# Kernel tuning notes

Measured on AMD Instinct MI355X. Metric: run time of the kernel, lower is better.

The kernel has to match this reference:

```python
import jax, jax.numpy as jnp
import numpy as np

B, S, D = 8, 1024, 768
H = 12
HD = D // H
DROPOUT_P = 0.5


def setup_inputs() -> dict:
    key = jax.random.key(0)
    ks = jax.random.split(key, 9)
    scale = 1.0 / np.sqrt(D)
    return {
        "x": jax.random.normal(ks[0], (B, S, D), dtype=jnp.float32),
        "wq": jax.random.normal(ks[1], (D, D), dtype=jnp.float32) * scale,
        "bq": jax.random.normal(ks[2], (D,), dtype=jnp.float32) * 0.01,
        "wk": jax.random.normal(ks[3], (D, D), dtype=jnp.float32) * scale,
        "bk": jax.random.normal(ks[4], (D,), dtype=jnp.float32) * 0.01,
        "wv": jax.random.normal(ks[5], (D, D), dtype=jnp.float32) * scale,
        "bv": jax.random.normal(ks[6], (D,), dtype=jnp.float32) * 0.01,
        "wo": jax.random.normal(ks[7], (D, D), dtype=jnp.float32) * scale,
        "bo": jax.random.normal(ks[8], (D,), dtype=jnp.float32) * 0.01,
    }


def reference(x, wq, bq, wk, bk, wv, bv, wo, bo):
    # QKV projections (torch Linear: y = x @ W.T + b)
    def proj(w, b):
        y = jnp.einsum("bsd,ed->bse", x, w) + b
        # [B,S,D] -> [B,H,S,HD]
        return y.reshape(B, S, H, HD).transpose(0, 2, 1, 3)

    q = proj(wq, bq)
    k = proj(wk, bk)
    v = proj(wv, bv)

    scores = jnp.einsum("bhqd,bhkd->bhqk", q, k) / jnp.sqrt(
        jnp.asarray(HD, dtype=x.dtype)
    )
    # dropout BEFORE softmax (non-standard, faithful to source), training=True
    dkey = jax.random.key(42)
    keep = jax.random.bernoulli(dkey, 1.0 - DROPOUT_P, scores.shape)
    scores = jnp.where(keep, scores / (1.0 - DROPOUT_P), 0.0)

    attn = jax.nn.softmax(scores, axis=-1)
    o = jnp.einsum("bhqk,bhkd->bhqd", attn, v)
    o = o.transpose(0, 2, 1, 3).reshape(B, S, D)
    return jnp.einsum("bsd,ed->bse", o, wo) + bo
```

## Files before the change

### kernel.cpp

```cpp
#include <hip/hip_runtime.h>
#include <hip/hip_bf16.h>
#include <stdint.h>

typedef __bf16 bf16_t;
typedef __attribute__((ext_vector_type(8))) __bf16 bf16x8;
typedef __attribute__((ext_vector_type(4))) __bf16 bf16x4;
typedef __attribute__((ext_vector_type(4))) float f32x4;

#define MFMA16(a, b, c) __builtin_amdgcn_mfma_f32_16x16x32_bf16(a, b, c, 0, 0, 0)

#define KS2 (0x1BD11BDAu ^ 42u)

__device__ __forceinline__ uint32_t mask_half16(uint32_t base) {
    const uint32_t bc = base + 42u;
    uint32_t p0 = 0u, p1 = 0u, p2 = 0u, p3 = 0u;

#define ROT4(rr)                                                        \
    {                                                                   \
        y00 += y10; y10 = __builtin_amdgcn_alignbit(y10, y10, 32u - (rr)); y10 ^= y00; \
        y01 += y11; y11 = __builtin_amdgcn_alignbit(y11, y11, 32u - (rr)); y11 ^= y01; \
        y02 += y12; y12 = __builtin_amdgcn_alignbit(y12, y12, 32u - (rr)); y12 ^= y02; \
        y03 += y13; y13 = __builtin_amdgcn_alignbit(y13, y13, 32u - (rr)); y13 ^= y03; \
    }
#define INJ4(a, b)                                                      \
    {                                                                   \
        y00 += (a); y10 += (b);                                         \
        y01 += (a); y11 += (b);                                         \
        y02 += (a); y12 += (b);                                         \
        y03 += (a); y13 += (b);                                         \
    }

#pragma unroll
    for (int c = 0; c < 16; c += 4) {
        uint32_t y00 = 0u, y10 = bc + (uint32_t)c;
        uint32_t y01 = 0u, y11 = bc + (uint32_t)(c + 1);
        uint32_t y02 = 0u, y12 = bc + (uint32_t)(c + 2);
        uint32_t y03 = 0u, y13 = bc + (uint32_t)(c + 3);

        ROT4(13) ROT4(15) ROT4(26) ROT4(6)   INJ4(42u, KS2 + 1u)
        ROT4(17) ROT4(29) ROT4(16) ROT4(24)  INJ4(KS2, 0u + 2u)
        ROT4(13) ROT4(15) ROT4(26) ROT4(6)   INJ4(0u, 42u + 3u)
        ROT4(17) ROT4(29) ROT4(16) ROT4(24)  INJ4(42u, KS2 + 4u)
        ROT4(13) ROT4(15) ROT4(26) ROT4(6)   INJ4(KS2, 0u + 5u)

        p0 |= ((y00 ^ y10) >> 31) << (c + 0);
        p1 |= ((y01 ^ y11) >> 31) << (c + 1);
        p2 |= ((y02 ^ y12) >> 31) << (c + 2);
        p3 |= ((y03 ^ y13) >> 31) << (c + 3);
    }
#undef ROT4
#undef INJ4
    return (p0 | p1) | (p2 | p3);
}

__device__ __forceinline__ bf16x8 cvt8(float4 a, float4 b) {
    bf16x8 v;
    v[0] = (bf16_t)a.x; v[1] = (bf16_t)a.y; v[2] = (bf16_t)a.z; v[3] = (bf16_t)a.w;
    v[4] = (bf16_t)b.x; v[5] = (bf16_t)b.y; v[6] = (bf16_t)b.z; v[7] = (bf16_t)b.w;
    return v;
}

__global__ __launch_bounds__(256, 2)
void qkv_gemm(const float* __restrict__ x,
              const float* __restrict__ wq, const float* __restrict__ bq,
              const float* __restrict__ wk, const float* __restrict__ bk,
              const float* __restrict__ wv, const float* __restrict__ bv,
              bf16_t* __restrict__ qb, bf16_t* __restrict__ kb, bf16_t* __restrict__ vtb)
{
    const int mt = blockIdx.x;
    const int nt = blockIdx.y;
    const int mat = blockIdx.z;
    const float* w   = (mat == 0) ? wq : ((mat == 1) ? wk : wv);
    const float* bia = (mat == 0) ? bq : ((mat == 1) ? bk : bv);

    __shared__ bf16_t As[128][40];
    __shared__ bf16_t Bs[128][40];

    const int t = threadIdx.x;
    const int wid = t >> 6, l = t & 63, l15 = l & 15, lg = l >> 4;
    const int wr = wid >> 1, wc = wid & 1;

    f32x4 acc[4][4] = {};

    const int srow = t >> 1, scol = (t & 1) * 16;
    const float* xa = x + (size_t)(mt * 128 + srow) * 768 + scol;
    const float* wa = w + (size_t)(nt * 128 + srow) * 768 + scol;

    for (int kt = 0; kt < 24; ++kt) {
        const float* pa = xa + kt * 32;
        const float* pb = wa + kt * 32;
        float4 a0 = *(const float4*)(pa + 0),  a1 = *(const float4*)(pa + 4);
        float4 a2 = *(const float4*)(pa + 8),  a3 = *(const float4*)(pa + 12);
        float4 b0 = *(const float4*)(pb + 0),  b1 = *(const float4*)(pb + 4);
        float4 b2 = *(const float4*)(pb + 8),  b3 = *(const float4*)(pb + 12);
        __syncthreads();
        *(bf16x8*)&As[srow][scol]     = cvt8(a0, a1);
        *(bf16x8*)&As[srow][scol + 8] = cvt8(a2, a3);
        *(bf16x8*)&Bs[srow][scol]     = cvt8(b0, b1);
        *(bf16x8*)&Bs[srow][scol + 8] = cvt8(b2, b3);
        __syncthreads();

        bf16x8 af[4], bf[4];
#pragma unroll
        for (int m = 0; m < 4; ++m) af[m] = *(const bf16x8*)&As[wr * 64 + m * 16 + l15][lg * 8];
#pragma unroll
        for (int n = 0; n < 4; ++n) bf[n] = *(const bf16x8*)&Bs[wc * 64 + n * 16 + l15][lg * 8];
#pragma unroll
        for (int m = 0; m < 4; ++m)
#pragma unroll
            for (int n = 0; n < 4; ++n)
                acc[m][n] = MFMA16(af[m], bf[n], acc[m][n]);
    }

    const int eb = nt * 128 + wc * 64;
    const int mb = mt * 128 + wr * 64;
#pragma unroll
    for (int n = 0; n < 4; ++n) {
        const int e = eb + n * 16 + l15;
        const float bias = bia[e];
        const int h = e >> 6, hd = e & 63;
#pragma unroll
        for (int m = 0; m < 4; ++m) {
            const int m0 = mb + m * 16 + lg * 4;
            const int b = m0 >> 10, s0 = m0 & 1023;
            if (mat == 2) {
                bf16x4 pv;
#pragma unroll
                for (int r = 0; r < 4; ++r) pv[r] = (bf16_t)(acc[m][n][r] + bias);
                *(bf16x4*)(vtb + (((size_t)(b * 12 + h)) << 16) + ((size_t)hd << 10) + s0) = pv;
            } else {
                bf16_t* dst = (mat == 0) ? qb : kb;
                const float sc = (mat == 0) ? 0.25f : 1.0f;
                const size_t base = (((size_t)(b * 12 + h)) << 16) + ((size_t)s0 << 6) + hd;
#pragma unroll
                for (int r = 0; r < 4; ++r)
                    dst[base + (size_t)r * 64] = (bf16_t)((acc[m][n][r] + bias) * sc);
            }
        }
    }
}

__global__ __launch_bounds__(512, 4)
void attn_kernel(const bf16_t* __restrict__ qb, const bf16_t* __restrict__ kb,
                 const bf16_t* __restrict__ vtb, bf16_t* __restrict__ ob)
{
    const int qt = blockIdx.x;
    const int bh = blockIdx.y;
    const int t = threadIdx.x, w = t >> 6, l = t & 63, l15 = l & 15, lg = l >> 4;

    __shared__ bf16_t Kl[2][64][72];
    __shared__ bf16_t Vl[2][64][72];
    __shared__ bf16_t Pl[4][16][72];
    __shared__ ushort Mh[2][64][2][2];

    const size_t base = ((size_t)bh) << 16;
    const uint32_t fbase = ((uint32_t)bh) << 20;
    const int q0b = qt * 64;

    const int q0 = q0b + w * 16;
    const int u = t & 255;
    const int mq = u >> 2, mword = (u >> 1) & 1, mhalf = u & 1;
    const uint32_t moff = (uint32_t)(mword * 32 + mhalf * 16);

    f32x4 oacc[4] = {};
    float mst[4], lst[4];
    bf16x8 qf[2];

    if (w < 4) {
        const size_t qbase = base + (size_t)(q0 + l15) * 64 + lg * 8;
        qf[0] = *(const bf16x8*)(qb + qbase);
        qf[1] = *(const bf16x8*)(qb + qbase + 32);
#pragma unroll
        for (int r = 0; r < 4; ++r) { mst[r] = -1e30f; lst[r] = 0.f; }
#pragma unroll
        for (int sdx = 0; sdx < 2; ++sdx) {
            const int idx = sdx * 256 + t;
            const int row = idx >> 3, seg = idx & 7;
            *(uint4*)&Kl[0][row][seg * 8] =
                *(const uint4*)(kb + base + ((size_t)row << 6) + seg * 8);
            *(uint4*)&Vl[0][row][seg * 8] =
                *(const uint4*)(vtb + base + ((size_t)row << 10) + seg * 8);
        }
    } else {
        const uint32_t mbase = fbase | ((uint32_t)(q0b + mq) << 10) | moff;
        Mh[0][mq][mword][mhalf] = (ushort)mask_half16(mbase);
    }
    __syncthreads();

    for (int kt = 0; kt < 16; ++kt) {
        const int cur = kt & 1, nxt = cur ^ 1;
        if (w < 4) {
            const int ktn = (kt < 15) ? kt + 1 : 15;
            const int row0 = t >> 3, seg = t & 7;
            const int row1 = row0 + 32;
            const uint4 ka0 = *(const uint4*)(kb + base + ((size_t)(ktn * 64 + row0) << 6) + seg * 8);
            const uint4 ka1 = *(const uint4*)(kb + base + ((size_t)(ktn * 64 + row1) << 6) + seg * 8);
            const uint4 va0 = *(const uint4*)(vtb + base + ((size_t)row0 << 10) + ktn * 64 + seg * 8);
            const uint4 va1 = *(const uint4*)(vtb + base + ((size_t)row1 << 10) + ktn * 64 + seg * 8);

            f32x4 sc[4] = {};
#pragma unroll
            for (int ks = 0; ks < 2; ++ks)
#pragma unroll
                for (int n = 0; n < 4; ++n) {
                    bf16x8 kf = *(const bf16x8*)&Kl[cur][n * 16 + l15][ks * 32 + lg * 8];
                    sc[n] = MFMA16(qf[ks], kf, sc[n]);
                }

#pragma unroll
            for (int r = 0; r < 4; ++r) {
                const int ql = w * 16 + lg * 4 + r;
                const uint32_t* mrow = (const uint32_t*)&Mh[cur][ql][0][0];
                const uint32_t w0 = mrow[0], w1 = mrow[1];
#pragma unroll
                for (int n = 0; n < 4; ++n) {
                    const uint32_t wrd = (n < 2) ? w0 : w1;
                    const uint32_t bit = ((uint32_t)(n & 1) << 4) + (uint32_t)l15;
                    if ((wrd >> bit) & 1u) sc[n][r] = 0.f;
                }
            }

#pragma unroll
            for (int r = 0; r < 4; ++r) {
                float tm = fmaxf(fmaxf(sc[0][r], sc[1][r]), fmaxf(sc[2][r], sc[3][r]));
#pragma unroll
                for (int mk = 1; mk < 16; mk <<= 1) tm = fmaxf(tm, __shfl_xor(tm, mk));
                const float mnew = fmaxf(mst[r], tm);
                const float corr = __expf(mst[r] - mnew);
                float ps = 0.f;
#pragma unroll
                for (int n = 0; n < 4; ++n) {
                    const float p = __expf(sc[n][r] - mnew);
                    ps += p;
                    Pl[w][lg * 4 + r][n * 16 + l15] = (bf16_t)p;
                }
#pragma unroll
                for (int mk = 1; mk < 16; mk <<= 1) ps += __shfl_xor(ps, mk);
                lst[r] = lst[r] * corr + ps;
                mst[r] = mnew;
#pragma unroll
                for (int n = 0; n < 4; ++n) oacc[n][r] *= corr;
            }

            {
                const bf16x8 pa0 = *(const bf16x8*)&Pl[w][l15][lg * 8];
                const bf16x8 pa1 = *(const bf16x8*)&Pl[w][l15][32 + lg * 8];
#pragma unroll
                for (int n = 0; n < 4; ++n) {
                    const bf16x8 v0 = *(const bf16x8*)&Vl[cur][n * 16 + l15][lg * 8];
                    const bf16x8 v1 = *(const bf16x8*)&Vl[cur][n * 16 + l15][32 + lg * 8];
                    oacc[n] = MFMA16(pa0, v0, oacc[n]);
                    oacc[n] = MFMA16(pa1, v1, oacc[n]);
                }
            }

            {
                const int row0w = t >> 3, segw = t & 7;
                *(uint4*)&Kl[nxt][row0w][segw * 8]      = ka0;
                *(uint4*)&Kl[nxt][row0w + 32][segw * 8] = ka1;
                *(uint4*)&Vl[nxt][row0w][segw * 8]      = va0;
                *(uint4*)&Vl[nxt][row0w + 32][segw * 8] = va1;
            }
        } else if (kt < 15) {
            const uint32_t mbase = fbase | ((uint32_t)(q0b + mq) << 10)
                                 | ((uint32_t)((kt + 1) * 64) + moff);
            Mh[nxt][mq][mword][mhalf] = (ushort)mask_half16(mbase);
        }
        __syncthreads();
    }

    if (w < 4) {
        const int b = bh / 12, h = bh % 12;
#pragma unroll
        for (int r = 0; r < 4; ++r) {
            const float inv = 1.f / lst[r];
            const size_t row = ((size_t)(b * 1024 + q0 + lg * 4 + r)) * 768 + h * 64;
#pragma unroll
            for (int n = 0; n < 4; ++n)
                ob[row + n * 16 + l15] = (bf16_t)(oacc[n][r] * inv);
        }
    }
}

__global__ __launch_bounds__(256, 2)
void out_gemm(const bf16_t* __restrict__ ob, const float* __restrict__ wo,
              const float* __restrict__ bo, float* __restrict__ out)
{
    const int mt = blockIdx.x, nt = blockIdx.y;
    __shared__ bf16_t As[128][40];
    __shared__ bf16_t Bs[128][40];
    const int t = threadIdx.x;
    const int wid = t >> 6, l = t & 63, l15 = l & 15, lg = l >> 4;
    const int wr = wid >> 1, wc = wid & 1;
    f32x4 acc[4][4] = {};

    const int srow = t >> 1, scol = (t & 1) * 16;
    const bf16_t* aa = ob + (size_t)(mt * 128 + srow) * 768 + scol;
    const float*  wa = wo + (size_t)(nt * 128 + srow) * 768 + scol;

    for (int kt = 0; kt < 24; ++kt) {
        uint4 a01 = *(const uint4*)(aa + kt * 32);
        uint4 a23 = *(const uint4*)(aa + kt * 32 + 8);
        const float* pb = wa + kt * 32;
        float4 b0 = *(const float4*)(pb + 0), b1 = *(const float4*)(pb + 4);
        float4 b2 = *(const float4*)(pb + 8), b3 = *(const float4*)(pb + 12);
        __syncthreads();
        *(uint4*)&As[srow][scol]      = a01;
        *(uint4*)&As[srow][scol + 8]  = a23;
        *(bf16x8*)&Bs[srow][scol]     = cvt8(b0, b1);
        *(bf16x8*)&Bs[srow][scol + 8] = cvt8(b2, b3);
        __syncthreads();

        bf16x8 af[4], bf[4];
#pragma unroll
        for (int m = 0; m < 4; ++m) af[m] = *(const bf16x8*)&As[wr * 64 + m * 16 + l15][lg * 8];
#pragma unroll
        for (int n = 0; n < 4; ++n) bf[n] = *(const bf16x8*)&Bs[wc * 64 + n * 16 + l15][lg * 8];
#pragma unroll
        for (int m = 0; m < 4; ++m)
#pragma unroll
            for (int n = 0; n < 4; ++n)
                acc[m][n] = MFMA16(af[m], bf[n], acc[m][n]);
    }

#pragma unroll
    for (int n = 0; n < 4; ++n) {
        const int e = nt * 128 + wc * 64 + n * 16 + l15;
        const float bias = bo[e];
#pragma unroll
        for (int m = 0; m < 4; ++m) {
            const int m0 = mt * 128 + wr * 64 + m * 16 + lg * 4;
#pragma unroll
            for (int r = 0; r < 4; ++r)
                out[(size_t)(m0 + r) * 768 + e] = acc[m][n][r] + bias;
        }
    }
}

__global__ void fill_zero(float* p, int n) {
    int i = blockIdx.x * 256 + threadIdx.x;
    if (i < n) p[i] = 0.f;
}

extern "C" void kernel_launch(void* const* d_in, const int* in_sizes, int n_in,
                              void* d_out, int out_size, void* d_ws, size_t ws_size,
                              hipStream_t stream) {
    const float* x  = (const float*)d_in[0];
    const float* wq = (const float*)d_in[1];
    const float* bq = (const float*)d_in[2];
    const float* wk = (const float*)d_in[3];
    const float* bk = (const float*)d_in[4];
    const float* wv = (const float*)d_in[5];
    const float* bv = (const float*)d_in[6];
    const float* wo = (const float*)d_in[7];
    const float* bo = (const float*)d_in[8];
    float* out = (float*)d_out;

    const size_t NEED = 4ull * 6291456ull * 2ull;
    if (ws_size < NEED) {
        fill_zero<<<(out_size + 255) / 256, 256, 0, stream>>>(out, out_size);
        return;
    }

    bf16_t* qb  = (bf16_t*)d_ws;
    bf16_t* kb  = qb  + 6291456;
    bf16_t* vtb = kb  + 6291456;
    bf16_t* ob  = vtb + 6291456;

    qkv_gemm<<<dim3(64, 6, 3), 256, 0, stream>>>(x, wq, bq, wk, bk, wv, bv, qb, kb, vtb);
    attn_kernel<<<dim3(16, 96), 512, 0, stream>>>(qb, kb, vtb, ob);
    out_gemm<<<dim3(64, 6), 256, 0, stream>>>(ob, wo, bo, out);
}
```

Measured before the change: 317.6 us.

## Precompute early dropout masks in QKV GEMM and drop online-softmax max tracking

Adds 256 extra threads to each QKV GEMM block. They generate the Threefry dropout mask words for the first key tiles into a global buffer while the MFMA waves run, using matching barrier counts. The attention kernel reads those words from global memory for the early tiles and only computes masks in its helper waves for the later tiles. Softmax no longer tracks a running max or rescales: it exponentiates scores directly and reduces the row sum once at the end. This removes shuffles and corrections but risks overflow if scores become large.

New measurement: 298.2 us. -6.1%, faster.

```diff
diff --git a/kernel.cpp b/kernel.cpp
--- a/kernel.cpp
+++ b/kernel.cpp
@@ -10,10 +10,8 @@
 #define MFMA16(a, b, c) __builtin_amdgcn_mfma_f32_16x16x32_bf16(a, b, c, 0, 0, 0)
 
 #define KS2 (0x1BD11BDAu ^ 42u)
-
-__device__ __forceinline__ uint32_t mask_half16(uint32_t base) {
-    const uint32_t bc = base + 42u;
-    uint32_t p0 = 0u, p1 = 0u, p2 = 0u, p3 = 0u;
+#define OFF_TILES 6
+#define GMASK_WORDS 1179648u
 
 #define ROT4(rr)                                                        \
     {                                                                   \
@@ -30,27 +28,26 @@
         y03 += (a); y13 += (b);                                         \
     }
 
-#pragma unroll
-    for (int c = 0; c < 16; c += 4) {
-        uint32_t y00 = 0u, y10 = bc + (uint32_t)c;
-        uint32_t y01 = 0u, y11 = bc + (uint32_t)(c + 1);
-        uint32_t y02 = 0u, y12 = bc + (uint32_t)(c + 2);
-        uint32_t y03 = 0u, y13 = bc + (uint32_t)(c + 3);
-
-        ROT4(13) ROT4(15) ROT4(26) ROT4(6)   INJ4(42u, KS2 + 1u)
-        ROT4(17) ROT4(29) ROT4(16) ROT4(24)  INJ4(KS2, 0u + 2u)
-        ROT4(13) ROT4(15) ROT4(26) ROT4(6)   INJ4(0u, 42u + 3u)
-        ROT4(17) ROT4(29) ROT4(16) ROT4(24)  INJ4(42u, KS2 + 4u)
-        ROT4(13) ROT4(15) ROT4(26) ROT4(6)   INJ4(KS2, 0u + 5u)
-
-        p0 |= ((y00 ^ y10) >> 31) << (c + 0);
-        p1 |= ((y01 ^ y11) >> 31) << (c + 1);
-        p2 |= ((y02 ^ y12) >> 31) << (c + 2);
-        p3 |= ((y03 ^ y13) >> 31) << (c + 3);
-    }
-#undef ROT4
-#undef INJ4
-    return (p0 | p1) | (p2 | p3);
+__device__ __forceinline__ uint32_t tf4bits(uint32_t e0, int c) {
+    uint32_t y00 = 0u, y10 = e0 + 42u;
+    uint32_t y01 = 0u, y11 = e0 + 43u;
+    uint32_t y02 = 0u, y12 = e0 + 44u;
+    uint32_t y03 = 0u, y13 = e0 + 45u;
+    ROT4(13) ROT4(15) ROT4(26) ROT4(6)   INJ4(42u, KS2 + 1u)
+    ROT4(17) ROT4(29) ROT4(16) ROT4(24)  INJ4(KS2, 0u + 2u)
+    ROT4(13) ROT4(15) ROT4(26) ROT4(6)   INJ4(0u, 42u + 3u)
+    ROT4(17) ROT4(29) ROT4(16) ROT4(24)  INJ4(42u, KS2 + 4u)
+    ROT4(13) ROT4(15) ROT4(26) ROT4(6)   INJ4(KS2, 0u + 5u)
+    const uint32_t b0 = (y00 ^ y10) >> 31, b1 = (y01 ^ y11) >> 31;
+    const uint32_t b2 = (y02 ^ y12) >> 31, b3 = (y03 ^ y13) >> 31;
+    return (b0 | (b1 << 1) | (b2 << 2) | (b3 << 3)) << c;
+}
+
+__device__ __forceinline__ uint32_t mask_half16(uint32_t base) {
+    uint32_t r = 0u;
+#pragma unroll
+    for (int c = 0; c < 16; c += 4) r |= tf4bits(base + (uint32_t)c, c);
+    return r;
 }
 
 __device__ __forceinline__ bf16x8 cvt8(float4 a, float4 b) {
@@ -60,89 +57,118 @@
     return v;
 }
 
-__global__ __launch_bounds__(256, 2)
+__global__ __launch_bounds__(512, 4)
 void qkv_gemm(const float* __restrict__ x,
               const float* __restrict__ wq, const float* __restrict__ bq,
               const float* __restrict__ wk, const float* __restrict__ bk,
               const float* __restrict__ wv, const float* __restrict__ bv,
-              bf16_t* __restrict__ qb, bf16_t* __restrict__ kb, bf16_t* __restrict__ vtb)
+              bf16_t* __restrict__ qb, bf16_t* __restrict__ kb,
+              bf16_t* __restrict__ vtb, uint32_t* __restrict__ gmask)
 {
     const int mt = blockIdx.x;
     const int nt = blockIdx.y;
     const int mat = blockIdx.z;
-    const float* w   = (mat == 0) ? wq : ((mat == 1) ? wk : wv);
-    const float* bia = (mat == 0) ? bq : ((mat == 1) ? bk : bv);
 
     __shared__ bf16_t As[128][40];
     __shared__ bf16_t Bs[128][40];
 
     const int t = threadIdx.x;
-    const int wid = t >> 6, l = t & 63, l15 = l & 15, lg = l >> 4;
-    const int wr = wid >> 1, wc = wid & 1;
-
-    f32x4 acc[4][4] = {};
-
-    const int srow = t >> 1, scol = (t & 1) * 16;
-    const float* xa = x + (size_t)(mt * 128 + srow) * 768 + scol;
-    const float* wa = w + (size_t)(nt * 128 + srow) * 768 + scol;
-
-    for (int kt = 0; kt < 24; ++kt) {
-        const float* pa = xa + kt * 32;
-        const float* pb = wa + kt * 32;
-        float4 a0 = *(const float4*)(pa + 0),  a1 = *(const float4*)(pa + 4);
-        float4 a2 = *(const float4*)(pa + 8),  a3 = *(const float4*)(pa + 12);
-        float4 b0 = *(const float4*)(pb + 0),  b1 = *(const float4*)(pb + 4);
-        float4 b2 = *(const float4*)(pb + 8),  b3 = *(const float4*)(pb + 12);
-        __syncthreads();
-        *(bf16x8*)&As[srow][scol]     = cvt8(a0, a1);
-        *(bf16x8*)&As[srow][scol + 8] = cvt8(a2, a3);
-        *(bf16x8*)&Bs[srow][scol]     = cvt8(b0, b1);
-        *(bf16x8*)&Bs[srow][scol + 8] = cvt8(b2, b3);
-        __syncthreads();
-
-        bf16x8 af[4], bf[4];
-#pragma unroll
-        for (int m = 0; m < 4; ++m) af[m] = *(const bf16x8*)&As[wr * 64 + m * 16 + l15][lg * 8];
-#pragma unroll
-        for (int n = 0; n < 4; ++n) bf[n] = *(const bf16x8*)&Bs[wc * 64 + n * 16 + l15][lg * 8];
-#pragma unroll
-        for (int m = 0; m < 4; ++m)
-#pragma unroll
-            for (int n = 0; n < 4; ++n)
-                acc[m][n] = MFMA16(af[m], bf[n], acc[m][n]);
-    }
-
-    const int eb = nt * 128 + wc * 64;
-    const int mb = mt * 128 + wr * 64;
-#pragma unroll
-    for (int n = 0; n < 4; ++n) {
-        const int e = eb + n * 16 + l15;
-        const float bias = bia[e];
-        const int h = e >> 6, hd = e & 63;
-#pragma unroll
-        for (int m = 0; m < 4; ++m) {
-            const int m0 = mb + m * 16 + lg * 4;
-            const int b = m0 >> 10, s0 = m0 & 1023;
-            if (mat == 2) {
-                bf16x4 pv;
-#pragma unroll
-                for (int r = 0; r < 4; ++r) pv[r] = (bf16_t)(acc[m][n][r] + bias);
-                *(bf16x4*)(vtb + (((size_t)(b * 12 + h)) << 16) + ((size_t)hd << 10) + s0) = pv;
-            } else {
-                bf16_t* dst = (mat == 0) ? qb : kb;
-                const float sc = (mat == 0) ? 0.25f : 1.0f;
-                const size_t base = (((size_t)(b * 12 + h)) << 16) + ((size_t)s0 << 6) + hd;
-#pragma unroll
-                for (int r = 0; r < 4; ++r)
-                    dst[base + (size_t)r * 64] = (bf16_t)((acc[m][n][r] + bias) * sc);
-            }
+
+    if (t < 256) {
+        const float* w   = (mat == 0) ? wq : ((mat == 1) ? wk : wv);
+        const float* bia = (mat == 0) ? bq : ((mat == 1) ? bk : bv);
+        const int wid = t >> 6, l = t & 63, l15 = l & 15, lg = l >> 4;
+        const int wr = wid >> 1, wc = wid & 1;
+
+        f32x4 acc[4][4] = {};
+        const int srow = t >> 1, scol = (t & 1) * 16;
+        const float* xa = x + (size_t)(mt * 128 + srow) * 768 + scol;
+        const float* wa = w + (size_t)(nt * 128 + srow) * 768 + scol;
+
+        for (int kt = 0; kt < 24; ++kt) {
+            const float* pa = xa + kt * 32;
+            const float* pb = wa + kt * 32;
+            float4 a0 = *(const float4*)(pa + 0),  a1 = *(const float4*)(pa + 4);
+            float4 a2 = *(const float4*)(pa + 8),  a3 = *(const float4*)(pa + 12);
+            float4 b0 = *(const float4*)(pb + 0),  b1 = *(const float4*)(pb + 4);
+            float4 b2 = *(const float4*)(pb + 8),  b3 = *(const float4*)(pb + 12);
+            __syncthreads();
+            *(bf16x8*)&As[srow][scol]     = cvt8(a0, a1);
+            *(bf16x8*)&As[srow][scol + 8] = cvt8(a2, a3);
+            *(bf16x8*)&Bs[srow][scol]     = cvt8(b0, b1);
+            *(bf16x8*)&Bs[srow][scol + 8] = cvt8(b2, b3);
+            __syncthreads();
+
+            bf16x8 af[4], bf[4];
+#pragma unroll
+            for (int m = 0; m < 4; ++m) af[m] = *(const bf16x8*)&As[wr * 64 + m * 16 + l15][lg * 8];
+#pragma unroll
+            for (int n = 0; n < 4; ++n) bf[n] = *(const bf16x8*)&Bs[wc * 64 + n * 16 + l15][lg * 8];
+#pragma unroll
+            for (int m = 0; m < 4; ++m)
+#pragma unroll
+                for (int n = 0; n < 4; ++n)
+                    acc[m][n] = MFMA16(af[m], bf[n], acc[m][n]);
+        }
+
+        const int eb = nt * 128 + wc * 64;
+        const int mb = mt * 128 + wr * 64;
+#pragma unroll
+        for (int n = 0; n < 4; ++n) {
+            const int e = eb + n * 16 + l15;
+            const float bias = bia[e];
+            const int h = e >> 6, hd = e & 63;
+#pragma unroll
+            for (int m = 0; m < 4; ++m) {
+                const int m0 = mb + m * 16 + lg * 4;
+                const int b = m0 >> 10, s0 = m0 & 1023;
+                if (mat == 2) {
+                    bf16x4 pv;
+#pragma unroll
+                    for (int r = 0; r < 4; ++r) pv[r] = (bf16_t)(acc[m][n][r] + bias);
+                    *(bf16x4*)(vtb + (((size_t)(b * 12 + h)) << 16) + ((size_t)hd << 10) + s0) = pv;
+                } else {
+                    bf16_t* dst = (mat == 0) ? qb : kb;
+                    const float sc = (mat == 0) ? 0.25f : 1.0f;
+                    const size_t base = (((size_t)(b * 12 + h)) << 16) + ((size_t)s0 << 6) + hd;
+#pragma unroll
+                    for (int r = 0; r < 4; ++r)
+                        dst[base + (size_t)r * 64] = (bf16_t)((acc[m][n][r] + bias) * sc);
+                }
+            }
+        }
+    } else {
+        const uint32_t u = (uint32_t)(t - 256);
+        const uint32_t bl = (uint32_t)(mt + 64 * (nt + 6 * mat));
+        const uint32_t wbase = bl * 1024u + u;
+        uint32_t word = 0u, ebase = 0u, widx = 0u;
+        int s = 0;
+        for (int it = 0; it < 24; ++it) {
+            const int nseg = (it < 8) ? 2 : 1;
+            for (int q2 = 0; q2 < nseg; ++q2, ++s) {
+                const int chunk = s >> 3, c = (s & 7) * 4;
+                if ((s & 7) == 0) {
+                    widx = wbase + 256u * (uint32_t)chunk;
+                    const uint32_t bh  = widx / 12288u;
+                    const uint32_t rem = widx - bh * 12288u;
+                    const uint32_t q   = rem / 12u;
+                    const uint32_t w12 = rem - q * 12u;
+                    ebase = (bh << 20) | (q << 10) | (w12 * 32u);
+                    word = 0u;
+                }
+                word |= tf4bits(ebase + (uint32_t)c, c);
+                if ((s & 7) == 7) gmask[widx] = word;
+            }
+            __syncthreads();
+            __syncthreads();
         }
     }
 }
 
 __global__ __launch_bounds__(512, 4)
 void attn_kernel(const bf16_t* __restrict__ qb, const bf16_t* __restrict__ kb,
-                 const bf16_t* __restrict__ vtb, bf16_t* __restrict__ ob)
+                 const bf16_t* __restrict__ vtb, const uint32_t* __restrict__ gmask,
+                 bf16_t* __restrict__ ob)
 {
     const int qt = blockIdx.x;
     const int bh = blockIdx.y;
@@ -156,22 +182,20 @@
     const size_t base = ((size_t)bh) << 16;
     const uint32_t fbase = ((uint32_t)bh) << 20;
     const int q0b = qt * 64;
-
     const int q0 = q0b + w * 16;
+
     const int u = t & 255;
     const int mq = u >> 2, mword = (u >> 1) & 1, mhalf = u & 1;
     const uint32_t moff = (uint32_t)(mword * 32 + mhalf * 16);
 
     f32x4 oacc[4] = {};
-    float mst[4], lst[4];
+    float lst[4] = {0.f, 0.f, 0.f, 0.f};
     bf16x8 qf[2];
 
     if (w < 4) {
         const size_t qbase = base + (size_t)(q0 + l15) * 64 + lg * 8;
         qf[0] = *(const bf16x8*)(qb + qbase);
         qf[1] = *(const bf16x8*)(qb + qbase + 32);
-#pragma unroll
-        for (int r = 0; r < 4; ++r) { mst[r] = -1e30f; lst[r] = 0.f; }
 #pragma unroll
         for (int sdx = 0; sdx < 2; ++sdx) {
             const int idx = sdx * 256 + t;
@@ -181,9 +205,6 @@
             *(uint4*)&Vl[0][row][seg * 8] =
                 *(const uint4*)(vtb + base + ((size_t)row << 10) + seg * 8);
         }
-    } else {
-        const uint32_t mbase = fbase | ((uint32_t)(q0b + mq) << 10) | moff;
-        Mh[0][mq][mword][mhalf] = (ushort)mask_half16(mbase);
     }
     __syncthreads();
 
@@ -210,36 +231,26 @@
 #pragma unroll
             for (int r = 0; r < 4; ++r) {
                 const int ql = w * 16 + lg * 4 + r;
-                const uint32_t* mrow = (const uint32_t*)&Mh[cur][ql][0][0];
-                const uint32_t w0 = mrow[0], w1 = mrow[1];
+                uint32_t w0, w1;
+                if (kt < OFF_TILES) {
+                    const uint32_t qg = (uint32_t)(q0b + ql);
+                    const uint32_t wi = ((uint32_t)bh * 1024u + qg) * 12u + (uint32_t)(kt * 2);
+                    w0 = gmask[wi]; w1 = gmask[wi + 1];
+                } else {
+                    const uint32_t* mrow = (const uint32_t*)&Mh[cur][ql][0][0];
+                    w0 = mrow[0]; w1 = mrow[1];
+                }
+                float ps = 0.f;
 #pragma unroll
                 for (int n = 0; n < 4; ++n) {
                     const uint32_t wrd = (n < 2) ? w0 : w1;
                     const uint32_t bit = ((uint32_t)(n & 1) << 4) + (uint32_t)l15;
-                    if ((wrd >> bit) & 1u) sc[n][r] = 0.f;
-                }
-            }
-
-#pragma unroll
-            for (int r = 0; r < 4; ++r) {
-                float tm = fmaxf(fmaxf(sc[0][r], sc[1][r]), fmaxf(sc[2][r], sc[3][r]));
-#pragma unroll
-                for (int mk = 1; mk < 16; mk <<= 1) tm = fmaxf(tm, __shfl_xor(tm, mk));
-                const float mnew = fmaxf(mst[r], tm);
-                const float corr = __expf(mst[r] - mnew);
-                float ps = 0.f;
-#pragma unroll
-                for (int n = 0; n < 4; ++n) {
-                    const float p = __expf(sc[n][r] - mnew);
+                    const float e = __expf(sc[n][r]);
+                    const float p = ((wrd >> bit) & 1u) ? 1.0f : e;
                     ps += p;
                     Pl[w][lg * 4 + r][n * 16 + l15] = (bf16_t)p;
                 }
-#pragma unroll
-                for (int mk = 1; mk < 16; mk <<= 1) ps += __shfl_xor(ps, mk);
-                lst[r] = lst[r] * corr + ps;
-                mst[r] = mnew;
-#pragma unroll
-                for (int n = 0; n < 4; ++n) oacc[n][r] *= corr;
+                lst[r] += ps;
             }
 
             {
@@ -261,7 +272,7 @@
                 *(uint4*)&Vl[nxt][row0w][segw * 8]      = va0;
                 *(uint4*)&Vl[nxt][row0w + 32][segw * 8] = va1;
             }
-        } else if (kt < 15) {
+        } else if (kt >= OFF_TILES - 1 && kt < 15) {
             const uint32_t mbase = fbase | ((uint32_t)(q0b + mq) << 10)
                                  | ((uint32_t)((kt + 1) * 64) + moff);
             Mh[nxt][mq][mword][mhalf] = (ushort)mask_half16(mbase);
@@ -273,7 +284,10 @@
         const int b = bh / 12, h = bh % 12;
 #pragma unroll
         for (int r = 0; r < 4; ++r) {
-            const float inv = 1.f / lst[r];
+            float ps = lst[r];
+#pragma unroll
+            for (int mk = 1; mk < 16; mk <<= 1) ps += __shfl_xor(ps, mk);
+            const float inv = 1.f / ps;
             const size_t row = ((size_t)(b * 1024 + q0 + lg * 4 + r)) * 768 + h * 64;
 #pragma unroll
             for (int n = 0; n < 4; ++n)
@@ -356,7 +370,7 @@
     const float* bo = (const float*)d_in[8];
     float* out = (float*)d_out;
 
-    const size_t NEED = 4ull * 6291456ull * 2ull;
+    const size_t NEED = 4ull * 6291456ull * 2ull + (size_t)GMASK_WORDS * 4ull;
     if (ws_size < NEED) {
         fill_zero<<<(out_size + 255) / 256, 256, 0, stream>>>(out, out_size);
         return;
@@ -366,8 +380,10 @@
     bf16_t* kb  = qb  + 6291456;
     bf16_t* vtb = kb  + 6291456;
     bf16_t* ob  = vtb + 6291456;
-
-    qkv_gemm<<<dim3(64, 6, 3), 256, 0, stream>>>(x, wq, bq, wk, bk, wv, bv, qb, kb, vtb);
-    attn_kernel<<<dim3(16, 96), 512, 0, stream>>>(qb, kb, vtb, ob);
+    uint32_t* gmask = (uint32_t*)(ob + 6291456);
+
+    qkv_gemm<<<dim3(64, 6, 3), 512, 0, stream>>>(x, wq, bq, wk, bk, wv, bv,
+                                                 qb, kb, vtb, gmask);
+    attn_kernel<<<dim3(16, 96), 512, 0, stream>>>(qb, kb, vtb, gmask, ob);
     out_gemm<<<dim3(64, 6), 256, 0, stream>>>(ob, wo, bo, out);
 }
```
